# Kernel optimization log

Measured on AMD Instinct MI355X. Metric: run time of the kernel, lower is better.

## Reference

```python
import jax, jax.numpy as jnp
import numpy as np

N_NODES = 50000
N_EDGES = 1600000
NODE_DIM = 64
HID = 16


def setup_inputs() -> dict:
    key = jax.random.key(0)
    ks = jax.random.split(key, 12)
    f = lambda k, shape: (jax.random.normal(k, shape, dtype=jnp.float32) * 0.1)
    edge_index = jax.random.randint(ks[0], (2, N_EDGES), 0, N_NODES)
    return {
        "edge_index": edge_index,
        "node_emb": f(ks[1], (N_NODES, NODE_DIM)),
        "edge_emb": f(ks[2], (N_EDGES, HID)),
        "W1": f(ks[3], (NODE_DIM, HID)),
        "att_src1": f(ks[4], (HID,)),
        "att_dst1": f(ks[5], (HID,)),
        "b1": jnp.zeros((HID,), jnp.float32),
        "W2": f(ks[6], (HID, HID)),
        "att_src2": f(ks[7], (HID,)),
        "att_dst2": f(ks[8], (HID,)),
        "b2": jnp.zeros((HID,), jnp.float32),
        "Wm1": f(ks[9], (3 * HID, HID)),
        "bm1": jnp.zeros((HID,), jnp.float32),
        "Wm2": f(ks[10], (HID, 1)),
        "bm2": jnp.zeros((1,), jnp.float32),
    }


def gat_layer(x, src, dst, W, a_src, a_dst, b, num_nodes):
    # Single-head GATConv (PyG defaults): self-loops, leaky_relu(0.2), softmax over dst.
    h = x @ W  # [N, out]
    logits = jax.nn.leaky_relu((h @ a_src)[src] + (h @ a_dst)[dst], negative_slope=0.2)
    m = jax.ops.segment_max(logits, dst, num_segments=num_nodes)  # stable softmax
    e = jnp.exp(logits - jax.lax.stop_gradient(m)[dst])
    denom = jax.ops.segment_sum(e, dst, num_segments=num_nodes)
    coef = e / denom[dst]  # [E+N]
    out = jax.ops.segment_sum(coef[:, None] * h[src], dst, num_segments=num_nodes)
    return out + b


def reference(edge_index, node_emb, edge_emb, W1, att_src1, att_dst1, b1,
              W2, att_src2, att_dst2, b2, Wm1, bm1, Wm2, bm2):
    src, dst = edge_index[0], edge_index[1]
    num_nodes = node_emb.shape[0]
    loops = jnp.arange(num_nodes)
    src_f = jnp.concatenate([src, loops])  # GATConv add_self_loops=True
    dst_f = jnp.concatenate([dst, loops])

    x = node_emb
    for (W, a_s, a_d, b) in [(W1, att_src1, att_dst1, b1), (W2, att_src2, att_dst2, b2)]:
        x = gat_layer(x, src_f, dst_f, W, a_s, a_d, b, num_nodes)
        x = jax.nn.gelu(x, approximate=False)  # torch F.gelu default = exact erf
        # dropout omitted (eval mode)

    # Vectorized replacement of the per-edge Python loop:
    edge_repr = jnp.concatenate([x[src], x[dst], edge_emb], axis=1)  # [E, 3*HID]
    hmid = jax.nn.relu(edge_repr @ Wm1 + bm1)
    probs = jax.nn.sigmoid(hmid @ Wm2 + bm2)[:, 0]  # [E]
    return probs
```

## Files before the change

kernel.cpp:

```cpp
#include <hip/hip_runtime.h>
#include <math.h>

#define N_NODES 50000
#define N_EDGES 1600000
#define NODE_DIM 64
#define HID 16
#define BSZ 64
#define NBUCK ((N_NODES + BSZ - 1) / BSZ)
#define CAPB 2560
#define EPB 2048
#define APB 256
#define APPEND_BLOCKS ((N_EDGES + EPB - 1) / EPB)

typedef _Float16 h8 __attribute__((ext_vector_type(8)));

__global__ void append_kernel(const int* __restrict__ ei,
                              int* __restrict__ gcount,
                              unsigned int* __restrict__ blist) {
    __shared__ int lcount[NBUCK];
    __shared__ int gbase[NBUCK];
    __shared__ int loff[NBUCK];
    int t = threadIdx.x;
    for (int b = t; b < NBUCK; b += APB) { lcount[b] = 0; loff[b] = 0; }
    __syncthreads();
    long base = (long)blockIdx.x * EPB;
#pragma unroll
    for (int k = 0; k < EPB / APB; k++) {
        long i = base + k * APB + t;
        if (i < N_EDGES) atomicAdd(&lcount[ei[N_EDGES + i] >> 6], 1);
    }
    __syncthreads();
    for (int b = t; b < NBUCK; b += APB) {
        int c = lcount[b];
        gbase[b] = c ? atomicAdd(&gcount[b], c) : 0;
    }
    __syncthreads();
#pragma unroll
    for (int k = 0; k < EPB / APB; k++) {
        long i = base + k * APB + t;
        if (i < N_EDGES) {
            int s = ei[i], d = ei[N_EDGES + i];
            int b = d >> 6;
            int pos = gbase[b] + atomicAdd(&loff[b], 1);
            if (pos < CAPB)
                blist[(size_t)b * CAPB + pos] = ((unsigned)(d & 63) << 16) | (unsigned)s;
        }
    }
}

__global__ void sort_kernel(const int* __restrict__ gcount, const unsigned int* __restrict__ blist,
                            unsigned short* __restrict__ csr, int* __restrict__ dstbeg) {
    __shared__ int cnts[BSZ];
    __shared__ int sc[BSZ];
    __shared__ int off[BSZ];
    int b = blockIdx.x, t = threadIdx.x;
    if (t < BSZ) cnts[t] = 0;
    __syncthreads();
    int cnt = gcount[b]; if (cnt > CAPB) cnt = CAPB;
    const unsigned int* lp = blist + (size_t)b * CAPB;
    for (int k = t; k < cnt; k += APB) atomicAdd(&cnts[lp[k] >> 16], 1);
    __syncthreads();
    if (t < BSZ) sc[t] = cnts[t];
    __syncthreads();
    for (int o = 1; o < BSZ; o <<= 1) {
        int v = 0;
        if (t < BSZ && t >= o) v = sc[t - o];
        __syncthreads();
        if (t < BSZ) sc[t] += v;
        __syncthreads();
    }
    if (t < BSZ) {
        int beg = sc[t] - cnts[t];
        off[t] = beg;
        dstbeg[(b << 6) + t] = beg;
    }
    __syncthreads();
    for (int k = t; k < cnt; k += APB) {
        unsigned int r = lp[k];
        int pos = atomicAdd(&off[r >> 16], 1);
        csr[(size_t)b * CAPB + pos] = (unsigned short)(r & 0xFFFF);
    }
}

__global__ void node_h64(const float* __restrict__ x,
                         const float* __restrict__ W,
                         const float* __restrict__ a_src,
                         const float* __restrict__ a_dst,
                         float* __restrict__ h,
                         float* __restrict__ as_, float* __restrict__ ad_) {
    __shared__ float Ws[NODE_DIM * HID];
    __shared__ float asv[HID], adv[HID];
    int t = threadIdx.x;
    for (int i = t; i < NODE_DIM * HID; i += blockDim.x) Ws[i] = W[i];
    if (t < HID) { asv[t] = a_src[t]; adv[t] = a_dst[t]; }
    __syncthreads();
    int n = blockIdx.x * blockDim.x + t;
    if (n >= N_NODES) return;
    float acc[HID];
#pragma unroll
    for (int j = 0; j < HID; j++) acc[j] = 0.f;
    const float4* xr = (const float4*)(x + (size_t)n * NODE_DIM);
#pragma unroll
    for (int k4 = 0; k4 < NODE_DIM / 4; k4++) {
        float4 xv = xr[k4];
        const float* w0 = Ws + (k4 * 4) * HID;
#pragma unroll
        for (int j = 0; j < HID; j++)
            acc[j] += xv.x * w0[j] + xv.y * w0[HID + j] + xv.z * w0[2 * HID + j] + xv.w * w0[3 * HID + j];
    }
    float s = 0.f, d = 0.f;
#pragma unroll
    for (int j = 0; j < HID; j++) {
        h[(size_t)n * HID + j] = acc[j];
        s += acc[j] * asv[j];
        d += acc[j] * adv[j];
    }
    as_[n] = s; ad_[n] = d;
}

__global__ void gather1_fused(const int* __restrict__ gcount, const int* __restrict__ dstbeg,
                              const unsigned short* __restrict__ csr,
                              const float* __restrict__ h,
                              const float* __restrict__ as_, const float* __restrict__ ad_,
                              const float* __restrict__ b,
                              const float* __restrict__ W2,
                              const float* __restrict__ a_src2,
                              const float* __restrict__ a_dst2,
                              float* __restrict__ h2out,
                              float* __restrict__ as2, float* __restrict__ ad2) {
    __shared__ float Ws[HID * HID];
    __shared__ float asv[HID], adv[HID], bs[HID];
    int t = threadIdx.x;
    for (int i = t; i < HID * HID; i += blockDim.x) Ws[i] = W2[i];
    if (t < HID) { asv[t] = a_src2[t]; adv[t] = a_dst2[t]; bs[t] = b[t]; }
    __syncthreads();
    int j = t & 15;
    float Wcol[HID];
#pragma unroll
    for (int k = 0; k < HID; k++) Wcol[k] = Ws[k * HID + j];
    float a2j = asv[j], d2j = adv[j], bj = bs[j];
    int g = blockIdx.x * (blockDim.x >> 4) + (t >> 4);
    if (g >= N_NODES) return;
    int bk = g >> 6, dl = g & 63;
    int cnt_b = gcount[bk]; if (cnt_b > CAPB) cnt_b = CAPB;
    int beg = dstbeg[g];
    int end = (dl < 63) ? dstbeg[g + 1] : cnt_b;
    if (end > cnt_b) end = cnt_b;
    if (beg > end) beg = end;
    const unsigned short* row = csr + (size_t)bk * CAPB + beg;
    int cnt = end - beg;
    float adn = ad_[g];
    float acc = 0.f, den = 0.f;
    int k = 0;
    for (; k + 4 <= cnt; k += 4) {
        int s0 = row[k], s1 = row[k + 1], s2 = row[k + 2], s3 = row[k + 3];
        float l0 = as_[s0] + adn, l1 = as_[s1] + adn;
        float l2 = as_[s2] + adn, l3 = as_[s3] + adn;
        l0 = l0 > 0.f ? l0 : 0.2f * l0;
        l1 = l1 > 0.f ? l1 : 0.2f * l1;
        l2 = l2 > 0.f ? l2 : 0.2f * l2;
        l3 = l3 > 0.f ? l3 : 0.2f * l3;
        float e0 = expf(l0), e1 = expf(l1), e2 = expf(l2), e3 = expf(l3);
        float h0 = h[(size_t)s0 * HID + j], h1 = h[(size_t)s1 * HID + j];
        float h2 = h[(size_t)s2 * HID + j], h3 = h[(size_t)s3 * HID + j];
        den += (e0 + e1) + (e2 + e3);
        acc += (e0 * h0 + e1 * h1) + (e2 * h2 + e3 * h3);
    }
    for (; k < cnt; k++) {
        int s = row[k];
        float lg = as_[s] + adn;
        lg = lg > 0.f ? lg : 0.2f * lg;
        float e = expf(lg);
        den += e;
        acc += e * h[(size_t)s * HID + j];
    }
    float lg = as_[g] + adn;
    lg = lg > 0.f ? lg : 0.2f * lg;
    float e = expf(lg);
    den += e;
    acc += e * h[(size_t)g * HID + j];
    float v = acc / den + bj;
    v = 0.5f * v * (1.f + erff(v * 0.70710678118654752f));
    float acc2 = 0.f;
#pragma unroll
    for (int k2 = 0; k2 < HID; k2++) {
        float xk = __shfl(v, k2, 16);
        acc2 += xk * Wcol[k2];
    }
    h2out[(size_t)g * HID + j] = acc2;
    float ps = acc2 * a2j, pd = acc2 * d2j;
#pragma unroll
    for (int o = 1; o < 16; o <<= 1) {
        ps += __shfl_xor(ps, o, 16);
        pd += __shfl_xor(pd, o, 16);
    }
    if (j == 0) { as2[g] = ps; ad2[g] = pd; }
}

__global__ void gather2_fused(const int* __restrict__ gcount, const int* __restrict__ dstbeg,
                              const unsigned short* __restrict__ csr,
                              const float* __restrict__ h,
                              const float* __restrict__ as_, const float* __restrict__ ad_,
                              const float* __restrict__ b,
                              const float* __restrict__ Wm1,
                              const float* __restrict__ bm1,
                              _Float16* __restrict__ A, _Float16* __restrict__ B) {
    __shared__ float Wa[HID * HID];
    __shared__ float Wb[HID * HID];
    __shared__ float bs[HID], b1s[HID];
    int t = threadIdx.x;
    for (int i = t; i < HID * HID; i += blockDim.x) {
        Wa[i] = Wm1[i];
        Wb[i] = Wm1[HID * HID + i];
    }
    if (t < HID) { bs[t] = b[t]; b1s[t] = bm1[t]; }
    __syncthreads();
    int j = t & 15;
    float WaC[HID], WbC[HID];
#pragma unroll
    for (int k = 0; k < HID; k++) { WaC[k] = Wa[k * HID + j]; WbC[k] = Wb[k * HID + j]; }
    float bj = bs[j], b1j = b1s[j];
    int g = blockIdx.x * (blockDim.x >> 4) + (t >> 4);
    if (g >= N_NODES) return;
    int bk = g >> 6, dl = g & 63;
    int cnt_b = gcount[bk]; if (cnt_b > CAPB) cnt_b = CAPB;
    int beg = dstbeg[g];
    int end = (dl < 63) ? dstbeg[g + 1] : cnt_b;
    if (end > cnt_b) end = cnt_b;
    if (beg > end) beg = end;
    const unsigned short* row = csr + (size_t)bk * CAPB + beg;
    int cnt = end - beg;
    float adn = ad_[g];
    float acc = 0.f, den = 0.f;
    int k = 0;
    for (; k + 4 <= cnt; k += 4) {
        int s0 = row[k], s1 = row[k + 1], s2 = row[k + 2], s3 = row[k + 3];
        float l0 = as_[s0] + adn, l1 = as_[s1] + adn;
        float l2 = as_[s2] + adn, l3 = as_[s3] + adn;
        l0 = l0 > 0.f ? l0 : 0.2f * l0;
        l1 = l1 > 0.f ? l1 : 0.2f * l1;
        l2 = l2 > 0.f ? l2 : 0.2f * l2;
        l3 = l3 > 0.f ? l3 : 0.2f * l3;
        float e0 = expf(l0), e1 = expf(l1), e2 = expf(l2), e3 = expf(l3);
        float h0 = h[(size_t)s0 * HID + j], h1 = h[(size_t)s1 * HID + j];
        float h2 = h[(size_t)s2 * HID + j], h3 = h[(size_t)s3 * HID + j];
        den += (e0 + e1) + (e2 + e3);
        acc += (e0 * h0 + e1 * h1) + (e2 * h2 + e3 * h3);
    }
    for (; k < cnt; k++) {
        int s = row[k];
        float lg = as_[s] + adn;
        lg = lg > 0.f ? lg : 0.2f * lg;
        float e = expf(lg);
        den += e;
        acc += e * h[(size_t)s * HID + j];
    }
    float lg = as_[g] + adn;
    lg = lg > 0.f ? lg : 0.2f * lg;
    float e = expf(lg);
    den += e;
    acc += e * h[(size_t)g * HID + j];
    float v = acc / den + bj;
    v = 0.5f * v * (1.f + erff(v * 0.70710678118654752f));
    float accA = b1j, accB = 0.f;
#pragma unroll
    for (int k2 = 0; k2 < HID; k2++) {
        float xk = __shfl(v, k2, 16);
        accA += xk * WaC[k2];
        accB += xk * WbC[k2];
    }
    A[(size_t)g * HID + j] = (_Float16)accA;
    B[(size_t)g * HID + j] = (_Float16)accB;
}

__global__ void edge_mlp(const int* __restrict__ ei,
                         const _Float16* __restrict__ A,
                         const _Float16* __restrict__ B,
                         const float* __restrict__ ee,
                         const float* __restrict__ Wm1,
                         const float* __restrict__ Wm2,
                         const float* __restrict__ bm2,
                         float* __restrict__ out) {
    __shared__ float We[HID * HID];
    __shared__ float W2s[HID];
    __shared__ float b2s;
    int t = threadIdx.x;
    for (int i = t; i < HID * HID; i += blockDim.x) We[i] = Wm1[2 * HID * HID + i];
    if (t < HID) W2s[t] = Wm2[t];
    if (t == 0) b2s = bm2[0];
    __syncthreads();
    long i = (long)blockIdx.x * blockDim.x + t;
    if (i >= N_EDGES) return;
    int s = ei[i], d = ei[N_EDGES + i];
    const h8* Ap = (const h8*)(A + (size_t)s * HID);
    const h8* Bp = (const h8*)(B + (size_t)d * HID);
    h8 a0 = Ap[0], a1 = Ap[1];
    h8 b0 = Bp[0], b1 = Bp[1];
    const float4* ep = (const float4*)(ee + (size_t)i * HID);
    float4 e0 = ep[0], e1 = ep[1], e2 = ep[2], e3 = ep[3];
    float a[HID];
#pragma unroll
    for (int j = 0; j < 8; j++) {
        a[j]     = (float)a0[j] + (float)b0[j];
        a[8 + j] = (float)a1[j] + (float)b1[j];
    }
    float ev[HID];
    ev[0]  = e0.x; ev[1]  = e0.y; ev[2]  = e0.z; ev[3]  = e0.w;
    ev[4]  = e1.x; ev[5]  = e1.y; ev[6]  = e1.z; ev[7]  = e1.w;
    ev[8]  = e2.x; ev[9]  = e2.y; ev[10] = e2.z; ev[11] = e2.w;
    ev[12] = e3.x; ev[13] = e3.y; ev[14] = e3.z; ev[15] = e3.w;
    const float4* W4 = (const float4*)We;
#pragma unroll
    for (int k = 0; k < HID; k++) {
        float e1v = ev[k];
        float4 w0 = W4[k * 4 + 0], w1 = W4[k * 4 + 1], w2 = W4[k * 4 + 2], w3 = W4[k * 4 + 3];
        a[0]  += e1v * w0.x; a[1]  += e1v * w0.y; a[2]  += e1v * w0.z; a[3]  += e1v * w0.w;
        a[4]  += e1v * w1.x; a[5]  += e1v * w1.y; a[6]  += e1v * w1.z; a[7]  += e1v * w1.w;
        a[8]  += e1v * w2.x; a[9]  += e1v * w2.y; a[10] += e1v * w2.z; a[11] += e1v * w2.w;
        a[12] += e1v * w3.x; a[13] += e1v * w3.y; a[14] += e1v * w3.z; a[15] += e1v * w3.w;
    }
    float o = b2s;
#pragma unroll
    for (int j = 0; j < HID; j++) o += fmaxf(a[j], 0.f) * W2s[j];
    out[i] = 1.f / (1.f + expf(-o));
}

extern "C" void kernel_launch(void* const* d_in, const int* in_sizes, int n_in,
                              void* d_out, int out_size, void* d_ws, size_t ws_size,
                              hipStream_t stream) {
    const int*   ei       = (const int*)d_in[0];
    const float* node_emb = (const float*)d_in[1];
    const float* edge_emb = (const float*)d_in[2];
    const float* W1       = (const float*)d_in[3];
    const float* att_src1 = (const float*)d_in[4];
    const float* att_dst1 = (const float*)d_in[5];
    const float* b1       = (const float*)d_in[6];
    const float* W2       = (const float*)d_in[7];
    const float* att_src2 = (const float*)d_in[8];
    const float* att_dst2 = (const float*)d_in[9];
    const float* b2       = (const float*)d_in[10];
    const float* Wm1      = (const float*)d_in[11];
    const float* bm1      = (const float*)d_in[12];
    const float* Wm2      = (const float*)d_in[13];
    const float* bm2      = (const float*)d_in[14];
    float* out            = (float*)d_out;

    char* w = (char*)d_ws;
    float*          h      = (float*)w;          w += (size_t)N_NODES * HID * 4;
    float*          h2     = (float*)w;          w += (size_t)N_NODES * HID * 4;
    float*          as_    = (float*)w;          w += (size_t)N_NODES * 4;
    float*          ad_    = (float*)w;          w += (size_t)N_NODES * 4;
    int*            gcount = (int*)w;            w += (size_t)NBUCK * 4;
    unsigned int*   blist  = (unsigned int*)w;   w += (size_t)NBUCK * CAPB * 4;
    unsigned short* csr    = (unsigned short*)w; w += (size_t)NBUCK * CAPB * 2;
    int*            dstbeg = (int*)w;            w += (size_t)NBUCK * BSZ * 4;

    _Float16* Anode = (_Float16*)blist;
    _Float16* Bnode = Anode + (size_t)N_NODES * HID;
    float*    as2   = (float*)(Bnode + (size_t)N_NODES * HID);
    float*    ad2   = as2 + N_NODES;

    const int BT = 256;
    int nblk_node = (N_NODES + BT - 1) / BT;
    int nblk_E    = (N_EDGES + BT - 1) / BT;
    int nblk_g    = (N_NODES * HID + BT - 1) / BT;

    hipMemsetAsync(gcount, 0, (size_t)NBUCK * sizeof(int), stream);
    append_kernel<<<APPEND_BLOCKS, APB, 0, stream>>>(ei, gcount, blist);
    sort_kernel<<<NBUCK, APB, 0, stream>>>(gcount, blist, csr, dstbeg);

    node_h64<<<nblk_node, BT, 0, stream>>>(node_emb, W1, att_src1, att_dst1, h, as_, ad_);
    gather1_fused<<<nblk_g, BT, 0, stream>>>(gcount, dstbeg, csr, h, as_, ad_, b1,
                                             W2, att_src2, att_dst2, h2, as2, ad2);

    gather2_fused<<<nblk_g, BT, 0, stream>>>(gcount, dstbeg, csr, h2, as2, ad2, b2,
                                             Wm1, bm1, Anode, Bnode);

    edge_mlp<<<nblk_E, BT, 0, stream>>>(ei, Anode, Bnode, edge_emb, Wm1, Wm2, bm2, out);
}
```

Measured before the change: 346.9 us.

## Split each node's edge gather across two half-groups and read weights directly

Result: slower. 355.1 us (+2.3%).

```diff
diff --git a/kernel.cpp b/kernel.cpp
--- a/kernel.cpp
+++ b/kernel.cpp
@@ -88,12 +88,7 @@
                          const float* __restrict__ a_dst,
                          float* __restrict__ h,
                          float* __restrict__ as_, float* __restrict__ ad_) {
-    __shared__ float Ws[NODE_DIM * HID];
-    __shared__ float asv[HID], adv[HID];
-    int t = threadIdx.x;
-    for (int i = t; i < NODE_DIM * HID; i += blockDim.x) Ws[i] = W[i];
-    if (t < HID) { asv[t] = a_src[t]; adv[t] = a_dst[t]; }
-    __syncthreads();
+    int t = threadIdx.x;
     int n = blockIdx.x * blockDim.x + t;
     if (n >= N_NODES) return;
     float acc[HID];
@@ -103,7 +98,7 @@
 #pragma unroll
     for (int k4 = 0; k4 < NODE_DIM / 4; k4++) {
         float4 xv = xr[k4];
-        const float* w0 = Ws + (k4 * 4) * HID;
+        const float* w0 = W + (k4 * 4) * HID;
 #pragma unroll
         for (int j = 0; j < HID; j++)
             acc[j] += xv.x * w0[j] + xv.y * w0[HID + j] + xv.z * w0[2 * HID + j] + xv.w * w0[3 * HID + j];
@@ -112,8 +107,8 @@
 #pragma unroll
     for (int j = 0; j < HID; j++) {
         h[(size_t)n * HID + j] = acc[j];
-        s += acc[j] * asv[j];
-        d += acc[j] * adv[j];
+        s += acc[j] * a_src[j];
+        d += acc[j] * a_dst[j];
     }
     as_[n] = s; ad_[n] = d;
 }
@@ -128,18 +123,14 @@
                               const float* __restrict__ a_dst2,
                               float* __restrict__ h2out,
                               float* __restrict__ as2, float* __restrict__ ad2) {
-    __shared__ float Ws[HID * HID];
-    __shared__ float asv[HID], adv[HID], bs[HID];
-    int t = threadIdx.x;
-    for (int i = t; i < HID * HID; i += blockDim.x) Ws[i] = W2[i];
-    if (t < HID) { asv[t] = a_src2[t]; adv[t] = a_dst2[t]; bs[t] = b[t]; }
-    __syncthreads();
+    int t = threadIdx.x;
     int j = t & 15;
+    int half = (t >> 4) & 1;
     float Wcol[HID];
 #pragma unroll
-    for (int k = 0; k < HID; k++) Wcol[k] = Ws[k * HID + j];
-    float a2j = asv[j], d2j = adv[j], bj = bs[j];
-    int g = blockIdx.x * (blockDim.x >> 4) + (t >> 4);
+    for (int k = 0; k < HID; k++) Wcol[k] = W2[k * HID + j];
+    float a2j = a_src2[j], d2j = a_dst2[j], bj = b[j];
+    int g = blockIdx.x * (blockDim.x >> 5) + (t >> 5);
     if (g >= N_NODES) return;
     int bk = g >> 6, dl = g & 63;
     int cnt_b = gcount[bk]; if (cnt_b > CAPB) cnt_b = CAPB;
@@ -149,10 +140,13 @@
     if (beg > end) beg = end;
     const unsigned short* row = csr + (size_t)bk * CAPB + beg;
     int cnt = end - beg;
+    int ch = (cnt + 1) >> 1;
+    int lo = half ? ch : 0;
+    int hi = half ? cnt : ch;
     float adn = ad_[g];
     float acc = 0.f, den = 0.f;
-    int k = 0;
-    for (; k + 4 <= cnt; k += 4) {
+    int k = lo;
+    for (; k + 4 <= hi; k += 4) {
         int s0 = row[k], s1 = row[k + 1], s2 = row[k + 2], s3 = row[k + 3];
         float l0 = as_[s0] + adn, l1 = as_[s1] + adn;
         float l2 = as_[s2] + adn, l3 = as_[s3] + adn;
@@ -166,7 +160,7 @@
         den += (e0 + e1) + (e2 + e3);
         acc += (e0 * h0 + e1 * h1) + (e2 * h2 + e3 * h3);
     }
-    for (; k < cnt; k++) {
+    for (; k < hi; k++) {
         int s = row[k];
         float lg = as_[s] + adn;
         lg = lg > 0.f ? lg : 0.2f * lg;
@@ -174,6 +168,8 @@
         den += e;
         acc += e * h[(size_t)s * HID + j];
     }
+    acc += __shfl_xor(acc, 16, 32);
+    den += __shfl_xor(den, 16, 32);
     float lg = as_[g] + adn;
     lg = lg > 0.f ? lg : 0.2f * lg;
     float e = expf(lg);
@@ -187,14 +183,16 @@
         float xk = __shfl(v, k2, 16);
         acc2 += xk * Wcol[k2];
     }
-    h2out[(size_t)g * HID + j] = acc2;
     float ps = acc2 * a2j, pd = acc2 * d2j;
 #pragma unroll
     for (int o = 1; o < 16; o <<= 1) {
         ps += __shfl_xor(ps, o, 16);
         pd += __shfl_xor(pd, o, 16);
     }
-    if (j == 0) { as2[g] = ps; ad2[g] = pd; }
+    if (half == 0) {
+        h2out[(size_t)g * HID + j] = acc2;
+        if (j == 0) { as2[g] = ps; ad2[g] = pd; }
+    }
 }
 
 __global__ void gather2_fused(const int* __restrict__ gcount, const int* __restrict__ dstbeg,
@@ -205,22 +203,17 @@
                               const float* __restrict__ Wm1,
                               const float* __restrict__ bm1,
                               _Float16* __restrict__ A, _Float16* __restrict__ B) {
-    __shared__ float Wa[HID * HID];
-    __shared__ float Wb[HID * HID];
-    __shared__ float bs[HID], b1s[HID];
-    int t = threadIdx.x;
-    for (int i = t; i < HID * HID; i += blockDim.x) {
-        Wa[i] = Wm1[i];
-        Wb[i] = Wm1[HID * HID + i];
-    }
-    if (t < HID) { bs[t] = b[t]; b1s[t] = bm1[t]; }
-    __syncthreads();
+    int t = threadIdx.x;
     int j = t & 15;
+    int half = (t >> 4) & 1;
     float WaC[HID], WbC[HID];
 #pragma unroll
-    for (int k = 0; k < HID; k++) { WaC[k] = Wa[k * HID + j]; WbC[k] = Wb[k * HID + j]; }
-    float bj = bs[j], b1j = b1s[j];
-    int g = blockIdx.x * (blockDim.x >> 4) + (t >> 4);
+    for (int k = 0; k < HID; k++) {
+        WaC[k] = Wm1[k * HID + j];
+        WbC[k] = Wm1[HID * HID + k * HID + j];
+    }
+    float bj = b[j], b1j = bm1[j];
+    int g = blockIdx.x * (blockDim.x >> 5) + (t >> 5);
     if (g >= N_NODES) return;
     int bk = g >> 6, dl = g & 63;
     int cnt_b = gcount[bk]; if (cnt_b > CAPB) cnt_b = CAPB;
@@ -230,10 +223,13 @@
     if (beg > end) beg = end;
     const unsigned short* row = csr + (size_t)bk * CAPB + beg;
     int cnt = end - beg;
+    int ch = (cnt + 1) >> 1;
+    int lo = half ? ch : 0;
+    int hi = half ? cnt : ch;
     float adn = ad_[g];
     float acc = 0.f, den = 0.f;
-    int k = 0;
-    for (; k + 4 <= cnt; k += 4) {
+    int k = lo;
+    for (; k + 4 <= hi; k += 4) {
         int s0 = row[k], s1 = row[k + 1], s2 = row[k + 2], s3 = row[k + 3];
         float l0 = as_[s0] + adn, l1 = as_[s1] + adn;
         float l2 = as_[s2] + adn, l3 = as_[s3] + adn;
@@ -247,7 +243,7 @@
         den += (e0 + e1) + (e2 + e3);
         acc += (e0 * h0 + e1 * h1) + (e2 * h2 + e3 * h3);
     }
-    for (; k < cnt; k++) {
+    for (; k < hi; k++) {
         int s = row[k];
         float lg = as_[s] + adn;
         lg = lg > 0.f ? lg : 0.2f * lg;
@@ -255,6 +251,8 @@
         den += e;
         acc += e * h[(size_t)s * HID + j];
     }
+    acc += __shfl_xor(acc, 16, 32);
+    den += __shfl_xor(den, 16, 32);
     float lg = as_[g] + adn;
     lg = lg > 0.f ? lg : 0.2f * lg;
     float e = expf(lg);
@@ -269,8 +267,10 @@
         accA += xk * WaC[k2];
         accB += xk * WbC[k2];
     }
-    A[(size_t)g * HID + j] = (_Float16)accA;
-    B[(size_t)g * HID + j] = (_Float16)accB;
+    if (half == 0) {
+        A[(size_t)g * HID + j] = (_Float16)accA;
+        B[(size_t)g * HID + j] = (_Float16)accB;
+    }
 }
 
 __global__ void edge_mlp(const int* __restrict__ ei,
@@ -281,14 +281,7 @@
                          const float* __restrict__ Wm2,
                          const float* __restrict__ bm2,
                          float* __restrict__ out) {
-    __shared__ float We[HID * HID];
-    __shared__ float W2s[HID];
-    __shared__ float b2s;
-    int t = threadIdx.x;
-    for (int i = t; i < HID * HID; i += blockDim.x) We[i] = Wm1[2 * HID * HID + i];
-    if (t < HID) W2s[t] = Wm2[t];
-    if (t == 0) b2s = bm2[0];
-    __syncthreads();
+    int t = threadIdx.x;
     long i = (long)blockIdx.x * blockDim.x + t;
     if (i >= N_EDGES) return;
     int s = ei[i], d = ei[N_EDGES + i];
@@ -309,7 +302,7 @@
     ev[4]  = e1.x; ev[5]  = e1.y; ev[6]  = e1.z; ev[7]  = e1.w;
     ev[8]  = e2.x; ev[9]  = e2.y; ev[10] = e2.z; ev[11] = e2.w;
     ev[12] = e3.x; ev[13] = e3.y; ev[14] = e3.z; ev[15] = e3.w;
-    const float4* W4 = (const float4*)We;
+    const float4* W4 = (const float4*)(Wm1 + 2 * HID * HID);
 #pragma unroll
     for (int k = 0; k < HID; k++) {
         float e1v = ev[k];
@@ -319,9 +312,9 @@
         a[8]  += e1v * w2.x; a[9]  += e1v * w2.y; a[10] += e1v * w2.z; a[11] += e1v * w2.w;
         a[12] += e1v * w3.x; a[13] += e1v * w3.y; a[14] += e1v * w3.z; a[15] += e1v * w3.w;
     }
-    float o = b2s;
-#pragma unroll
-    for (int j = 0; j < HID; j++) o += fmaxf(a[j], 0.f) * W2s[j];
+    float o = bm2[0];
+#pragma unroll
+    for (int j = 0; j < HID; j++) o += fmaxf(a[j], 0.f) * Wm2[j];
     out[i] = 1.f / (1.f + expf(-o));
 }
 
@@ -363,18 +356,18 @@
     const int BT = 256;
     int nblk_node = (N_NODES + BT - 1) / BT;
     int nblk_E    = (N_EDGES + BT - 1) / BT;
-    int nblk_g    = (N_NODES * HID + BT - 1) / BT;
+    int nblk_g32  = (N_NODES + (BT >> 5) - 1) / (BT >> 5);
 
     hipMemsetAsync(gcount, 0, (size_t)NBUCK * sizeof(int), stream);
     append_kernel<<<APPEND_BLOCKS, APB, 0, stream>>>(ei, gcount, blist);
     sort_kernel<<<NBUCK, APB, 0, stream>>>(gcount, blist, csr, dstbeg);
 
     node_h64<<<nblk_node, BT, 0, stream>>>(node_emb, W1, att_src1, att_dst1, h, as_, ad_);
-    gather1_fused<<<nblk_g, BT, 0, stream>>>(gcount, dstbeg, csr, h, as_, ad_, b1,
-                                             W2, att_src2, att_dst2, h2, as2, ad2);
-
-    gather2_fused<<<nblk_g, BT, 0, stream>>>(gcount, dstbeg, csr, h2, as2, ad2, b2,
-                                             Wm1, bm1, Anode, Bnode);
+    gather1_fused<<<nblk_g32, BT, 0, stream>>>(gcount, dstbeg, csr, h, as_, ad_, b1,
+                                               W2, att_src2, att_dst2, h2, as2, ad2);
+
+    gather2_fused<<<nblk_g32, BT, 0, stream>>>(gcount, dstbeg, csr, h2, as2, ad2, b2,
+                                               Wm1, bm1, Anode, Bnode);
 
     edge_mlp<<<nblk_E, BT, 0, stream>>>(ei, Anode, Bnode, edge_emb, Wm1, Wm2, bm2, out);
 }
```
